# Kernel optimization log

Measured on AMD Instinct MI355X. Metric: run time of the kernel, lower is better.

Reference implementation:

```python
import jax, jax.numpy as jnp
import numpy as np

B, S, D, H = 4, 2048, 512, 8
EPS = 1e-5


def setup_inputs() -> dict:
    key = jax.random.key(0)
    ks = jax.random.split(key, 8)
    s = lambda fan_in: 1.0 / np.sqrt(fan_in)
    return {
        "x": jax.random.normal(ks[0], (B, S, D), jnp.float32),
        "ln_w": jnp.ones((D,), jnp.float32),
        "ln_b": jnp.zeros((D,), jnp.float32),
        "q_w": jax.random.normal(ks[1], (D, D * H), jnp.float32) * s(D),
        "q_b": jnp.zeros((D * H,), jnp.float32),
        "k_w": jax.random.normal(ks[2], (D, D * H), jnp.float32) * s(D),
        "k_b": jnp.zeros((D * H,), jnp.float32),
        "v_w": jax.random.normal(ks[3], (D, D * H), jnp.float32) * s(D),
        "v_b": jnp.zeros((D * H,), jnp.float32),
        "o_w": jax.random.normal(ks[4], (D * H, D), jnp.float32) * s(D * H),
        "o_b": jnp.zeros((D,), jnp.float32),
    }


def reference(x, ln_w, ln_b, q_w, q_b, k_w, k_b, v_w, v_b, o_w, o_b):
    # LayerNorm over last dim
    mu = jnp.mean(x, axis=-1, keepdims=True)
    var = jnp.var(x, axis=-1, keepdims=True)
    xn = (x - mu) * jax.lax.rsqrt(var + EPS) * ln_w + ln_b

    def proj(w, b):  # [B,S,D] -> [B,H,S,D] (head_dim == D per the module)
        y = xn @ w + b
        return y.reshape(B, S, H, D).transpose(0, 2, 1, 3)

    q, k, v = proj(q_w, q_b), proj(k_w, k_b), proj(v_w, v_b)
    scale = D ** (-0.5)
    att = jnp.einsum("bhqd,bhkd->bhqk", q, k) * scale
    att = jax.nn.softmax(att, axis=-1)  # dropout p=0 -> identity
    out = jnp.einsum("bhqk,bhkd->bhqd", att, v)
    out = out.transpose(0, 2, 1, 3).reshape(B, S, H * D)
    return out @ o_w + o_b
```

## Files before the change

### kernel.cpp

```cpp
#include <hip/hip_runtime.h>

typedef unsigned short u16;
typedef unsigned int u32;
typedef long long i64;
typedef __attribute__((ext_vector_type(4))) float f32x4;
typedef __attribute__((ext_vector_type(8))) __bf16 bf16x8;

#define DEVI static __device__ __forceinline__

constexpr int kB = 4, kS = 2048, kD = 512, kH = 8;
constexpr int kND = kD * kH;
constexpr int kBS = kB * kS;
constexpr int kNQK = 2 * kND;
constexpr int kNQKV = 3 * kND;
constexpr float kScale = 0.044194173824159216f;

DEVI u16 f2bf(float f) {
  u32 u = __builtin_bit_cast(u32, f);
  return (u16)((u + 0x7fffu + ((u >> 16) & 1u)) >> 16);
}
DEVI float bf2f(u16 h) { return __builtin_bit_cast(float, (u32)h << 16); }

DEVI f32x4 mfma16(bf16x8 a, bf16x8 b, f32x4 c) {
  return __builtin_amdgcn_mfma_f32_16x16x32_bf16(a, b, c, 0, 0, 0);
}

DEVI void gld16(const u16* g, u16* l) {
  __builtin_amdgcn_global_load_lds(
      (const __attribute__((address_space(1))) void*)g,
      (__attribute__((address_space(3))) void*)l, 16, 0, 0);
}

__global__ void k_zero(float* __restrict__ p, int n) {
  int i = blockIdx.x * 256 + threadIdx.x;
  if (i < n) p[i] = 0.0f;
}

__global__ void k_cat2(const float* __restrict__ a, const float* __restrict__ b,
                       float* __restrict__ o) {
  int i = blockIdx.x * 256 + threadIdx.x;
  if (i < kND) o[i] = a[i];
  else if (i < 2 * kND) o[i] = b[i - kND];
}

__global__ __launch_bounds__(256) void k_red4(const float* __restrict__ p,
                                              const float* __restrict__ bias,
                                              float* __restrict__ out, int NP) {
  const int i = blockIdx.x * 256 + threadIdx.x;
  const float4* pv = reinterpret_cast<const float4*>(p);
  const float4 a = pv[i], b = pv[i + NP], c = pv[i + 2 * NP],
               d = pv[i + 3 * NP];
  const float4 bv = reinterpret_cast<const float4*>(bias)[i & 127];
  float4 r;
  r.x = a.x + b.x + c.x + d.x + bv.x;
  r.y = a.y + b.y + c.y + d.y + bv.y;
  r.z = a.z + b.z + c.z + d.z + bv.z;
  r.w = a.w + b.w + c.w + d.w + bv.w;
  reinterpret_cast<float4*>(out)[i] = r;
}

__global__ __launch_bounds__(256) void k_ln(const float* __restrict__ x,
                                            const float* __restrict__ lw,
                                            const float* __restrict__ lb,
                                            u16* __restrict__ xn) {
  const int lane = threadIdx.x & 63;
  const int row = (blockIdx.x << 2) + (threadIdx.x >> 6);
  const float4* xp = reinterpret_cast<const float4*>(x + (size_t)row * kD);
  float4 a = xp[lane * 2], b = xp[lane * 2 + 1];
  float s = a.x + a.y + a.z + a.w + b.x + b.y + b.z + b.w;
  float ss = a.x * a.x + a.y * a.y + a.z * a.z + a.w * a.w +
             b.x * b.x + b.y * b.y + b.z * b.z + b.w * b.w;
#pragma unroll
  for (int m = 1; m < 64; m <<= 1) {
    s += __shfl_xor(s, m, 64);
    ss += __shfl_xor(ss, m, 64);
  }
  const float mean = s * (1.0f / kD);
  const float var = ss * (1.0f / kD) - mean * mean;
  const float rstd = rsqrtf(fmaxf(var, 0.0f) + 1e-5f);
  const float4* wp = reinterpret_cast<const float4*>(lw);
  const float4* bp = reinterpret_cast<const float4*>(lb);
  float4 w0 = wp[lane * 2], w1 = wp[lane * 2 + 1];
  float4 b0 = bp[lane * 2], b1 = bp[lane * 2 + 1];
  float o0 = (a.x - mean) * rstd * w0.x + b0.x;
  float o1 = (a.y - mean) * rstd * w0.y + b0.y;
  float o2 = (a.z - mean) * rstd * w0.z + b0.z;
  float o3 = (a.w - mean) * rstd * w0.w + b0.w;
  float o4 = (b.x - mean) * rstd * w1.x + b1.x;
  float o5 = (b.y - mean) * rstd * w1.y + b1.y;
  float o6 = (b.z - mean) * rstd * w1.z + b1.z;
  float o7 = (b.w - mean) * rstd * w1.w + b1.w;
  uint4 st = make_uint4((u32)f2bf(o0) | ((u32)f2bf(o1) << 16),
                        (u32)f2bf(o2) | ((u32)f2bf(o3) << 16),
                        (u32)f2bf(o4) | ((u32)f2bf(o5) << 16),
                        (u32)f2bf(o6) | ((u32)f2bf(o7) << 16));
  *reinterpret_cast<uint4*>(xn + (size_t)row * kD + lane * 8) = st;
}

__global__ void k_wt(const float* __restrict__ in, u16* __restrict__ out,
                     int R, int C) {
  __shared__ float t[32][33];
  const int tx = threadIdx.x, ty = threadIdx.y;
  const int c0 = blockIdx.x << 5, r0 = blockIdx.y << 5;
#pragma unroll
  for (int i = 0; i < 4; i++)
    t[ty + 8 * i][tx] = in[(size_t)(r0 + ty + 8 * i) * C + c0 + tx];
  __syncthreads();
#pragma unroll
  for (int i = 0; i < 4; i++)
    out[(size_t)(c0 + ty + 8 * i) * R + r0 + tx] = f2bf(t[tx][ty + 8 * i]);
}

__global__ void k_vt(const u16* __restrict__ V, u16* __restrict__ VT, int ldv,
                     i64 sVz, i64 sVzH, i64 sTz) {
  const int z = blockIdx.z;
  V += (size_t)((i64)z * sVz + (i64)(z >> 3) * sVzH);
  VT += (size_t)((i64)z * sTz);
  __shared__ u16 t[32][33];
  const int tx = threadIdx.x, ty = threadIdx.y;
  const int s0 = blockIdx.x << 5, d0 = blockIdx.y << 5;
#pragma unroll
  for (int i = 0; i < 4; i++)
    t[ty + 8 * i][tx] = V[(size_t)(s0 + ty + 8 * i) * ldv + d0 + tx];
  __syncthreads();
#pragma unroll
  for (int i = 0; i < 4; i++)
    VT[(size_t)(d0 + ty + 8 * i) * kS + s0 + tx] = t[tx][ty + 8 * i];
}

template <int EPI, int BN>
DEVI void gemm_body(const u16* __restrict__ A, int lda, i64 sAz, i64 sAzH,
                    const u16* __restrict__ Bt, int ldb, i64 sBz, i64 sBzH,
                    void* __restrict__ Cb, int ldc, i64 sCz, i64 sCzH, int K,
                    const float* __restrict__ bias, float* __restrict__ lbase,
                    i64 sLz) {
  constexpr int NF = BN / 32;
  constexpr int BHALF = BN / 2;
  const int z = blockIdx.z;
  A += (size_t)((i64)z * sAz + (i64)(z >> 3) * sAzH);
  Bt += (size_t)((i64)z * sBz + (i64)(z >> 3) * sBzH);
  const i64 czoff = (i64)z * sCz + (i64)(z >> 3) * sCzH;
  float* lrow = lbase + (size_t)z * sLz;

  __shared__ __align__(16) u16 smem[8192 + 2 * BN * 32];
  u16* Asb = smem;
  u16* Bsb = smem + 8192;

  const int tid = threadIdx.x;
  const int lane = tid & 63, wid = tid >> 6;
  const int g = lane >> 4, lr = lane & 15;
  const int wr = wid >> 1, wc = wid & 1;
  const int m0 = blockIdx.x << 7, n0 = blockIdx.y * BN;

  const int scol = (((lane & 3) ^ ((lane >> 2) & 3)) << 3);
  const int srowA = (wid << 5) + (lane >> 2);
  const int srowB = (BN == 128) ? srowA : (wid << 4) + (lane >> 2);
  const u16* agp0 = A + (size_t)(m0 + srowA) * lda + scol;
  const u16* agp1 = A + (size_t)(m0 + srowA + 16) * lda + scol;
  const u16* bgp0 = Bt + (size_t)(n0 + srowB) * ldb + scol;
  const u16* bgp1 = Bt + (size_t)(n0 + srowB + 16) * ldb + scol;

  f32x4 acc[4][NF] = {};

  auto stage = [&](int ks, int buf) {
    const int ko = ks << 5;
    u16* ab = Asb + (buf << 12) + (wid << 10);
    gld16(agp0 + ko, ab);
    gld16(agp1 + ko, ab + 512);
    if constexpr (BN == 128) {
      u16* bb = Bsb + (buf << 12) + (wid << 10);
      gld16(bgp0 + ko, bb);
      gld16(bgp1 + ko, bb + 512);
    } else {
      u16* bb = Bsb + buf * (BN * 32) + (wid << 9);
      gld16(bgp0 + ko, bb);
    }
  };

  const int gx8 = ((g ^ (lr & 3)) << 3);

  const int nsteps = K >> 5;
  stage(0, 0);
  for (int ks = 0; ks < nsteps; ++ks) {
    const int cur = ks & 1;
    __syncthreads();
    if (ks + 1 < nsteps) stage(ks + 1, cur ^ 1);
    bf16x8 af[4], bfr[NF];
#pragma unroll
    for (int m = 0; m < 4; m++)
      af[m] = *reinterpret_cast<const bf16x8*>(
          &Asb[(cur << 12) + (wr * 64 + m * 16 + lr) * 32 + gx8]);
#pragma unroll
    for (int n = 0; n < NF; n++)
      bfr[n] = *reinterpret_cast<const bf16x8*>(
          &Bsb[cur * (BN * 32) + (wc * BHALF + n * 16 + lr) * 32 + gx8]);
#pragma unroll
    for (int m = 0; m < 4; m++)
#pragma unroll
      for (int n = 0; n < NF; n++)
        acc[m][n] = mfma16(af[m], bfr[n], acc[m][n]);
  }

  const int crow0 = m0 + wr * 64;
  const int ccol0 = n0 + wc * BHALF;

  if constexpr (EPI == 0) {
    u16* C16 = (u16*)Cb + (size_t)czoff;
#pragma unroll
    for (int n = 0; n < NF; n++) {
      const int col = ccol0 + n * 16 + lr;
      const float bv = bias[col];
#pragma unroll
      for (int m = 0; m < 4; m++)
#pragma unroll
        for (int j = 0; j < 4; j++) {
          const int row = crow0 + m * 16 + (g << 2) + j;
          C16[(size_t)row * ldc + col] = f2bf(acc[m][n][j] + bv);
        }
    }
  } else if constexpr (EPI == 1 || EPI == 4 || EPI == 6) {
    float* C32 = (float*)Cb + (size_t)czoff;
#pragma unroll
    for (int n = 0; n < NF; n++) {
      const int col = ccol0 + n * 16 + lr;
      const float bv = (EPI == 1) ? bias[col] : 0.0f;
#pragma unroll
      for (int m = 0; m < 4; m++)
#pragma unroll
        for (int j = 0; j < 4; j++) {
          const int row = crow0 + m * 16 + (g << 2) + j;
          float v = acc[m][n][j] + bv;
          if constexpr (EPI == 4) v += C32[(size_t)row * ldc + col];
          C32[(size_t)row * ldc + col] = v;
        }
    }
  } else if constexpr (EPI == 2) {
    u16* C16 = (u16*)Cb + (size_t)czoff;
#pragma unroll
    for (int m = 0; m < 4; m++) {
      float rsum[4] = {0.f, 0.f, 0.f, 0.f};
#pragma unroll
      for (int n = 0; n < NF; n++) {
        const int col = ccol0 + n * 16 + lr;
#pragma unroll
        for (int j = 0; j < 4; j++) {
          const float p = __expf(acc[m][n][j] * kScale);
          const u16 pb = f2bf(p);
          C16[(size_t)(crow0 + m * 16 + (g << 2) + j) * ldc + col] = pb;
          rsum[j] += bf2f(pb);
        }
      }
#pragma unroll
      for (int j = 0; j < 4; j++) {
        float r = rsum[j];
        r += __shfl_xor(r, 1, 64);
        r += __shfl_xor(r, 2, 64);
        r += __shfl_xor(r, 4, 64);
        r += __shfl_xor(r, 8, 64);
        if (lr == 0) atomicAdd(&lrow[crow0 + m * 16 + (g << 2) + j], r);
      }
    }
  } else if constexpr (EPI == 3) {
    u16* C16 = (u16*)Cb + (size_t)czoff;
#pragma unroll
    for (int m = 0; m < 4; m++)
#pragma unroll
      for (int j = 0; j < 4; j++) {
        const int row = crow0 + m * 16 + (g << 2) + j;
        const float inv = 1.0f / lrow[row];
#pragma unroll
        for (int n = 0; n < NF; n++) {
          const int col = ccol0 + n * 16 + lr;
          C16[(size_t)row * ldc + col] = f2bf(acc[m][n][j] * inv);
        }
      }
  } else if constexpr (EPI == 5) {
    u16* T = smem;
    __syncthreads();
#pragma unroll
    for (int n = 0; n < NF; n++) {
      const int cl = wc * BHALF + n * 16 + lr;
      const float bv = bias[n0 + cl];
#pragma unroll
      for (int m = 0; m < 4; m++) {
        const int rlb = wr * 64 + m * 16 + (g << 2);
#pragma unroll
        for (int j = 0; j < 4; j++) {
          const int rl = rlb + j;
          T[cl * 128 + ((((rl >> 3) ^ (cl & 7)) << 3) | (rl & 7))] =
              f2bf(acc[m][n][j] + bv);
        }
      }
    }
    __syncthreads();
    const int zb = ((m0 >> 11) << 3) + (n0 >> 9);
    u16* VT = (u16*)Cb + (size_t)zb * kD * kS + (size_t)(n0 & 511) * kS +
              (m0 & 2047);
#pragma unroll
    for (int p = 0; p < 8; p++) {
      const int dl = p * 16 + (tid >> 4);
      const int r8 = tid & 15;
      *reinterpret_cast<uint4*>(VT + (size_t)dl * kS + (r8 << 3)) =
          *reinterpret_cast<const uint4*>(
              &T[dl * 128 + ((r8 ^ (dl & 7)) << 3)]);
    }
  }
}

#define GEMM_ARGS                                                             \
  const u16 *A, int lda, i64 sAz, i64 sAzH, const u16 *Bt, int ldb, i64 sBz,  \
      i64 sBzH, void *Cb, int ldc, i64 sCz, i64 sCzH, int K,                  \
      const float *bias, float *lbase, i64 sLz
#define GEMM_PASS A, lda, sAz, sAzH, Bt, ldb, sBz, sBzH, Cb, ldc, sCz, sCzH, \
      K, bias, lbase, sLz

__global__ __launch_bounds__(256) void k_qkproj(GEMM_ARGS) {
  gemm_body<0, 128>(GEMM_PASS);
}
__global__ __launch_bounds__(256) void k_vproj(GEMM_ARGS) {
  gemm_body<5, 128>(GEMM_PASS);
}
__global__ __launch_bounds__(256) void k_qkt(GEMM_ARGS) {
  gemm_body<2, 128>(GEMM_PASS);
}
__global__ __launch_bounds__(256) void k_pv(GEMM_ARGS) {
  gemm_body<3, 64>(GEMM_PASS);
}
__global__ __launch_bounds__(256) void k_pv128(GEMM_ARGS) {
  gemm_body<3, 128>(GEMM_PASS);
}
__global__ __launch_bounds__(256) void k_osplit(GEMM_ARGS) {
  gemm_body<6, 64>(GEMM_PASS);
}
__global__ __launch_bounds__(256) void k_oproj(GEMM_ARGS) {
  gemm_body<1, 128>(GEMM_PASS);
}
__global__ __launch_bounds__(256) void k_oacc(GEMM_ARGS) {
  gemm_body<4, 128>(GEMM_PASS);
}

extern "C" void kernel_launch(void* const* d_in, const int* in_sizes, int n_in,
                              void* d_out, int out_size, void* d_ws,
                              size_t ws_size, hipStream_t stream) {
  const float* x = (const float*)d_in[0];
  const float* ln_w = (const float*)d_in[1];
  const float* ln_b = (const float*)d_in[2];
  const float* q_w = (const float*)d_in[3];
  const float* q_b = (const float*)d_in[4];
  const float* k_w = (const float*)d_in[5];
  const float* k_b = (const float*)d_in[6];
  const float* v_w = (const float*)d_in[7];
  const float* v_b = (const float*)d_in[8];
  const float* o_w = (const float*)d_in[9];
  const float* o_b = (const float*)d_in[10];
  float* out = (float*)d_out;

  constexpr size_t SZ_XN = (size_t)kBS * kD * 2;
  constexpr size_t SZ_QKVT = (size_t)kNQKV * kD * 2;
  constexpr size_t SZ_OWT = (size_t)kND * kD * 2;
  constexpr size_t SZ_CB = (size_t)kNQK * 4;
  constexpr size_t SZ_LB = (size_t)32 * kS * 4;
  constexpr size_t SZ_QK1 = (size_t)kS * kNQK * 2;
  constexpr size_t SZ_VT1 = (size_t)8 * kD * kS * 2;
  constexpr size_t SZ_S1 = (size_t)8 * kS * kS * 2;
  constexpr size_t SZ_TIER = SZ_QK1 + SZ_VT1 + SZ_S1;
  constexpr size_t SZ_AO = (size_t)kBS * kND * 2;
  constexpr size_t SZ_S = (size_t)kS * kS * 2;
  constexpr size_t SZ_H = (size_t)kBS * kD * 2;
  constexpr size_t SZ_BH = (size_t)kS * kD * 2;
  const size_t common = SZ_XN + SZ_QKVT + SZ_OWT + SZ_CB + SZ_LB;

  char* p = (char*)d_ws;
  auto alloc = [&](size_t bytes) {
    char* r = p;
    p += (bytes + 255) & ~(size_t)255;
    return r;
  };
  auto fits = [&](size_t extra) { return common + extra + 8192 <= ws_size; };

  int nb = 0, plan = -1, zc = 0;
  if (fits(4 * SZ_TIER)) nb = 4;
  else if (fits(2 * SZ_TIER)) nb = 2;
  else if (fits(1 * SZ_TIER)) nb = 1;
  else if (fits(4 * SZ_H + SZ_AO + 4 * SZ_S)) { plan = 1; zc = 4; }
  else if (fits(4 * SZ_H + SZ_AO + 1 * SZ_S)) { plan = 1; zc = 1; }
  else if (fits(5 * SZ_H + 4 * SZ_S)) { plan = 2; zc = 4; }
  else if (fits(5 * SZ_H + 1 * SZ_S)) { plan = 2; zc = 1; }
  else { plan = 3; zc = 1; }

  u16* xn = (u16*)alloc(SZ_XN);
  u16* qkvT = (u16*)alloc(SZ_QKVT);
  u16* owT = (u16*)alloc(SZ_OWT);
  float* cbias = (float*)alloc(SZ_CB);
  float* lbuf = (float*)alloc(SZ_LB);

  u16* kwT = qkvT + (size_t)kND * kD;
  u16* vwT = qkvT + (size_t)2 * kND * kD;

  k_zero<<<dim3(256), 256, 0, stream>>>(lbuf, 32 * kS);
  k_ln<<<dim3(kBS / 4), 256, 0, stream>>>(x, ln_w, ln_b, xn);
  dim3 tb(32, 8);
  k_wt<<<dim3(kND / 32, kD / 32), tb, 0, stream>>>(q_w, qkvT, kD, kND);
  k_wt<<<dim3(kND / 32, kD / 32), tb, 0, stream>>>(k_w, kwT, kD, kND);
  k_wt<<<dim3(kND / 32, kD / 32), tb, 0, stream>>>(v_w, vwT, kD, kND);
  k_wt<<<dim3(kD / 32, kND / 32), tb, 0, stream>>>(o_w, owT, kND, kD);

  const i64 sS = (i64)kS * kS;

  if (nb > 0) {
    u16* QKg = (u16*)alloc((size_t)nb * SZ_QK1);
    u16* VTg = (u16*)alloc((size_t)nb * SZ_VT1);
    u16* Sb = (u16*)alloc((size_t)nb * SZ_S1);
    u16* AOg = QKg;
    float* Pb = (float*)Sb;

    k_cat2<<<dim3(kNQK / 256), 256, 0, stream>>>(q_b, k_b, cbias);

    const i64 sHiA = (i64)kS * kNQK - 8 * kD;
    const i64 sHiAO = (i64)kS * kND - 8 * kD;
    const int zc8 = nb * 8;

    for (int g = 0; g < kB; g += nb) {
      const u16* xb = xn + (size_t)g * kS * kD;
      k_qkproj<<<dim3(nb * kS / 128, kNQK / 128), 256, 0, stream>>>(
          xb, kD, 0, 0, qkvT, kD, 0, 0, QKg, kNQK, 0, 0, kD, cbias, nullptr,
          0);
      k_vproj<<<dim3(nb * kS / 128, kND / 128), 256, 0, stream>>>(
          xb, kD, 0, 0, vwT, kD, 0, 0, VTg, 0, 0, 0, kD, v_b, nullptr, 0);

      float* lr0 = lbuf + (size_t)g * 8 * kS;
      k_qkt<<<dim3(16, 16, zc8), 256, 0, stream>>>(
          QKg, kNQK, kD, sHiA, QKg + kND, kNQK, kD, sHiA, Sb, kS, sS, 0, kD,
          nullptr, lr0, kS);
      k_pv128<<<dim3(16, 4, zc8), 256, 0, stream>>>(
          Sb, kS, sS, 0, VTg, kS, (i64)kD * kS, 0, AOg, kND, kD, sHiAO, kS,
          nullptr, lr0, kS);
      k_osplit<<<dim3(nb * kS / 128, kD / 64, 4), 256, 0, stream>>>(
          AOg, kND, 1024, 0, owT, kND, 1024, 0, Pb, kD, (i64)nb * kS * kD, 0,
          1024, nullptr, nullptr, 0);
      k_red4<<<dim3(nb * kS * kD / 4 / 256), 256, 0, stream>>>(
          Pb, o_b, out + (size_t)g * kS * kD, nb * kS * kD / 4);
    }
  } else if (plan == 1 || plan == 2) {
    u16* Qh = (u16*)alloc(SZ_H);
    u16* Kh = (u16*)alloc(SZ_H);
    u16* Vh = (u16*)alloc(SZ_H);
    u16* VTh = (u16*)alloc(SZ_H);
    u16* AO = (u16*)alloc(plan == 1 ? SZ_AO : SZ_H);
    u16* Sb = (u16*)alloc((size_t)zc * SZ_S);
    const int aold = (plan == 1) ? kND : kD;

    for (int h = 0; h < kH; h++) {
      const u16* qwh = qkvT + (size_t)h * kD * kD;
      const u16* kwh = kwT + (size_t)h * kD * kD;
      const u16* vwh = vwT + (size_t)h * kD * kD;
      k_qkproj<<<dim3(64, 4), 256, 0, stream>>>(xn, kD, 0, 0, qwh, kD, 0, 0,
                                                Qh, kD, 0, 0, kD, q_b + h * kD,
                                                nullptr, 0);
      k_qkproj<<<dim3(64, 4), 256, 0, stream>>>(xn, kD, 0, 0, kwh, kD, 0, 0,
                                                Kh, kD, 0, 0, kD, k_b + h * kD,
                                                nullptr, 0);
      k_qkproj<<<dim3(64, 4), 256, 0, stream>>>(xn, kD, 0, 0, vwh, kD, 0, 0,
                                                Vh, kD, 0, 0, kD, v_b + h * kD,
                                                nullptr, 0);
      k_vt<<<dim3(64, 16, 4), tb, 0, stream>>>(Vh, VTh, kD, (i64)kS * kD, 0,
                                               (i64)kD * kS);
      u16* AOh = (plan == 1) ? AO + (size_t)h * kD : AO;
      const i64 sAO = (plan == 1) ? (i64)kS * kND : (i64)kS * kD;
      for (int b0 = 0; b0 < kB; b0 += zc) {
        float* lr0 = lbuf + (size_t)(h * 4 + b0) * kS;
        k_qkt<<<dim3(16, 16, zc), 256, 0, stream>>>(
            Qh + (size_t)b0 * kS * kD, kD, (i64)kS * kD, 0,
            Kh + (size_t)b0 * kS * kD, kD, (i64)kS * kD, 0, Sb, kS, sS, 0, kD,
            nullptr, lr0, kS);
        k_pv<<<dim3(16, 8, zc), 256, 0, stream>>>(
            Sb, kS, sS, 0, VTh + (size_t)b0 * kD * kS, kS, (i64)kD * kS, 0,
            AOh + (size_t)b0 * kS * aold, aold, sAO, 0, kS, nullptr, lr0, kS);
      }
      if (plan == 2) {
        if (h == 0)
          k_oproj<<<dim3(64, 4), 256, 0, stream>>>(
              AO, kD, 0, 0, owT + (size_t)h * kD, kND, 0, 0, out, kD, 0, 0, kD,
              o_b, nullptr, 0);
        else
          k_oacc<<<dim3(64, 4), 256, 0, stream>>>(
              AO, kD, 0, 0, owT + (size_t)h * kD, kND, 0, 0, out, kD, 0, 0, kD,
              nullptr, nullptr, 0);
      }
    }
    if (plan == 1)
      k_oproj<<<dim3(64, 4), 256, 0, stream>>>(AO, kND, 0, 0, owT, kND, 0, 0,
                                               out, kD, 0, 0, kND, o_b,
                                               nullptr, 0);
  } else {
    u16* Qbh = (u16*)alloc(SZ_BH);
    u16* Kbh = (u16*)alloc(SZ_BH);
    u16* Vbh = (u16*)alloc(SZ_BH);
    u16* VTbh = (u16*)alloc(SZ_BH);
    u16* AObh = (u16*)alloc(SZ_BH);
    u16* Sb = (u16*)alloc(SZ_S);

    for (int b = 0; b < kB; b++)
      for (int h = 0; h < kH; h++) {
        const u16* xb = xn + (size_t)b * kS * kD;
        k_qkproj<<<dim3(16, 4), 256, 0, stream>>>(
            xb, kD, 0, 0, qkvT + (size_t)h * kD * kD, kD, 0, 0, Qbh, kD, 0, 0,
            kD, q_b + h * kD, nullptr, 0);
        k_qkproj<<<dim3(16, 4), 256, 0, stream>>>(
            xb, kD, 0, 0, kwT + (size_t)h * kD * kD, kD, 0, 0, Kbh, kD, 0, 0,
            kD, k_b + h * kD, nullptr, 0);
        k_qkproj<<<dim3(16, 4), 256, 0, stream>>>(
            xb, kD, 0, 0, vwT + (size_t)h * kD * kD, kD, 0, 0, Vbh, kD, 0, 0,
            kD, v_b + h * kD, nullptr, 0);
        k_vt<<<dim3(64, 16, 1), tb, 0, stream>>>(Vbh, VTbh, kD, 0, 0, 0);
        float* lr0 = lbuf + (size_t)(b * 8 + h) * kS;
        k_qkt<<<dim3(16, 16, 1), 256, 0, stream>>>(
            Qbh, kD, 0, 0, Kbh, kD, 0, 0, Sb, kS, 0, 0, kD, nullptr, lr0, 0);
        k_pv<<<dim3(16, 8, 1), 256, 0, stream>>>(
            Sb, kS, 0, 0, VTbh, kS, 0, 0, AObh, kD, 0, 0, kS, nullptr, lr0, 0);
        float* outb = out + (size_t)b * kS * kD;
        if (h == 0)
          k_oproj<<<dim3(16, 4), 256, 0, stream>>>(
              AObh, kD, 0, 0, owT, kND, 0, 0, outb, kD, 0, 0, kD, o_b, nullptr,
              0);
        else
          k_oacc<<<dim3(16, 4), 256, 0, stream>>>(
              AObh, kD, 0, 0, owT + (size_t)h * kD, kND, 0, 0, outb, kD, 0, 0,
              kD, nullptr, nullptr, 0);
      }
  }
}
```

Measured before the change: 686.1 us.

## Fuse Q/K/V projections into one launch and stage GEMM epilogues through LDS

Merges the separate QK and V projection kernels into a single GEMM launch over the concatenated QKV weight. Column tiles in the V range write a transposed V layout; the combined bias is built by a three-way concat kernel. The QK projection, QK^T/exp and PV epilogues now stage their bf16 tiles through swizzled shared memory and write 16-byte coalesced rows instead of scattered 2-byte stores. This adds extra barriers and LDS traffic in each epilogue, and it reuses the lbase argument to carry the VT pointer.

New measurement: 684.7 us. About the same (-0.2%).

```diff
diff --git a/kernel.cpp b/kernel.cpp
--- a/kernel.cpp
+++ b/kernel.cpp
@@ -36,11 +36,12 @@
   if (i < n) p[i] = 0.0f;
 }
 
-__global__ void k_cat2(const float* __restrict__ a, const float* __restrict__ b,
-                       float* __restrict__ o) {
+__global__ void k_cat3(const float* __restrict__ a, const float* __restrict__ b,
+                       const float* __restrict__ c, float* __restrict__ o) {
   int i = blockIdx.x * 256 + threadIdx.x;
   if (i < kND) o[i] = a[i];
   else if (i < 2 * kND) o[i] = b[i - kND];
+  else if (i < 3 * kND) o[i] = c[i - 2 * kND];
 }
 
 __global__ __launch_bounds__(256) void k_red4(const float* __restrict__ p,
@@ -128,6 +129,11 @@
     VT[(size_t)(d0 + ty + 8 * i) * kS + s0 + tx] = t[tx][ty + 8 * i];
 }
 
+DEVI int tidx(int row, int col) {
+  return row * 128 + ((((col >> 3) ^ (((row >> 2) & 3) << 1)) << 3) |
+                      (col & 7));
+}
+
 template <int EPI, int BN>
 DEVI void gemm_body(const u16* __restrict__ A, int lda, i64 sAz, i64 sAzH,
                     const u16* __restrict__ Bt, int ldb, i64 sBz, i64 sBzH,
@@ -204,19 +210,67 @@
   const int crow0 = m0 + wr * 64;
   const int ccol0 = n0 + wc * BHALF;
 
-  if constexpr (EPI == 0) {
-    u16* C16 = (u16*)Cb + (size_t)czoff;
-#pragma unroll
-    for (int n = 0; n < NF; n++) {
-      const int col = ccol0 + n * 16 + lr;
-      const float bv = bias[col];
-#pragma unroll
-      for (int m = 0; m < 4; m++)
-#pragma unroll
-        for (int j = 0; j < 4; j++) {
-          const int row = crow0 + m * 16 + (g << 2) + j;
-          C16[(size_t)row * ldc + col] = f2bf(acc[m][n][j] + bv);
+  auto flush128 = [&](u16* C16, int ld) {
+    __syncthreads();
+#pragma unroll
+    for (int it = 0; it < 8; ++it) {
+      const int r = it * 16 + (tid >> 4);
+      const int b = tid & 15;
+      const int sb = b ^ (((r >> 2) & 3) << 1);
+      *reinterpret_cast<uint4*>(C16 + (size_t)(m0 + r) * ld + n0 + b * 8) =
+          *reinterpret_cast<const uint4*>(&smem[r * 128 + sb * 8]);
+    }
+  };
+
+  if constexpr (EPI == 0 || EPI == 7) {
+    const bool qkpart = (EPI == 0) || (n0 < kNQK);
+    if (qkpart) {
+      __syncthreads();
+#pragma unroll
+      for (int n = 0; n < NF; n++) {
+        const int cl = wc * BHALF + n * 16 + lr;
+        const float bv = bias[n0 + cl];
+#pragma unroll
+        for (int m = 0; m < 4; m++)
+#pragma unroll
+          for (int j = 0; j < 4; j++) {
+            const int rl = wr * 64 + m * 16 + (g << 2) + j;
+            smem[tidx(rl, cl)] = f2bf(acc[m][n][j] + bv);
+          }
+      }
+      u16* C16 = (u16*)Cb + (size_t)czoff;
+      flush128(C16, ldc);
+    } else {
+      u16* T = smem;
+      __syncthreads();
+      const int ndl = n0 - kNQK;
+#pragma unroll
+      for (int n = 0; n < NF; n++) {
+        const int cl = wc * BHALF + n * 16 + lr;
+        const float bv = bias[n0 + cl];
+#pragma unroll
+        for (int m = 0; m < 4; m++) {
+          const int rlb = wr * 64 + m * 16 + (g << 2);
+#pragma unroll
+          for (int j = 0; j < 4; j++) {
+            const int rl = rlb + j;
+            T[cl * 128 + ((((rl >> 3) ^ (cl & 7)) << 3) | (rl & 7))] =
+                f2bf(acc[m][n][j] + bv);
+          }
         }
+      }
+      __syncthreads();
+      const int zb = ((m0 >> 11) << 3) + (ndl >> 9);
+      u16* VT = (u16*)lbase + (size_t)zb * kD * kS +
+                (size_t)(ndl & 511) * kS + (m0 & 2047);
+#pragma unroll
+      for (int p = 0; p < 8; p++) {
+        const int dl = p * 16 + (tid >> 4);
+        const int r8 = tid & 15;
+        *reinterpret_cast<uint4*>(VT + (size_t)dl * kS + (r8 << 3)) =
+            *reinterpret_cast<const uint4*>(
+                &T[dl * 128 + ((r8 ^ (dl & 7)) << 3)]);
+      }
     }
   } else if constexpr (EPI == 1 || EPI == 4 || EPI == 6) {
     float* C32 = (float*)Cb + (size_t)czoff;
@@ -235,18 +289,19 @@
         }
     }
   } else if constexpr (EPI == 2) {
-    u16* C16 = (u16*)Cb + (size_t)czoff;
+    __syncthreads();
 #pragma unroll
     for (int m = 0; m < 4; m++) {
       float rsum[4] = {0.f, 0.f, 0.f, 0.f};
 #pragma unroll
       for (int n = 0; n < NF; n++) {
-        const int col = ccol0 + n * 16 + lr;
+        const int cl = wc * BHALF + n * 16 + lr;
 #pragma unroll
         for (int j = 0; j < 4; j++) {
+          const int rl = wr * 64 + m * 16 + (g << 2) + j;
           const float p = __expf(acc[m][n][j] * kScale);
           const u16 pb = f2bf(p);
-          C16[(size_t)(crow0 + m * 16 + (g << 2) + j) * ldc + col] = pb;
+          smem[tidx(rl, cl)] = pb;
           rsum[j] += bf2f(pb);
         }
       }
@@ -260,49 +315,39 @@
         if (lr == 0) atomicAdd(&lrow[crow0 + m * 16 + (g << 2) + j], r);
       }
     }
+    u16* C16 = (u16*)Cb + (size_t)czoff;
+    flush128(C16, ldc);
   } else if constexpr (EPI == 3) {
-    u16* C16 = (u16*)Cb + (size_t)czoff;
-#pragma unroll
-    for (int m = 0; m < 4; m++)
-#pragma unroll
-      for (int j = 0; j < 4; j++) {
-        const int row = crow0 + m * 16 + (g << 2) + j;
-        const float inv = 1.0f / lrow[row];
-#pragma unroll
-        for (int n = 0; n < NF; n++) {
-          const int col = ccol0 + n * 16 + lr;
-          C16[(size_t)row * ldc + col] = f2bf(acc[m][n][j] * inv);
+    if constexpr (BN == 128) {
+      __syncthreads();
+#pragma unroll
+      for (int m = 0; m < 4; m++)
+#pragma unroll
+        for (int j = 0; j < 4; j++) {
+          const int rl = wr * 64 + m * 16 + (g << 2) + j;
+          const float inv = 1.0f / lrow[m0 + rl];
+#pragma unroll
+          for (int n = 0; n < NF; n++) {
+            const int cl = wc * BHALF + n * 16 + lr;
+            smem[tidx(rl, cl)] = f2bf(acc[m][n][j] * inv);
+          }
         }
-      }
-  } else if constexpr (EPI == 5) {
-    u16* T = smem;
-    __syncthreads();
-#pragma unroll
-    for (int n = 0; n < NF; n++) {
-      const int cl = wc * BHALF + n * 16 + lr;
-      const float bv = bias[n0 + cl];
-#pragma unroll
-      for (int m = 0; m < 4; m++) {
-        const int rlb = wr * 64 + m * 16 + (g << 2);
+      u16* C16 = (u16*)Cb + (size_t)czoff;
+      flush128(C16, ldc);
+    } else {
+      u16* C16 = (u16*)Cb + (size_t)czoff;
+#pragma unroll
+      for (int m = 0; m < 4; m++)
 #pragma unroll
         for (int j = 0; j < 4; j++) {
-          const int rl = rlb + j;
-          T[cl * 128 + ((((rl >> 3) ^ (cl & 7)) << 3) | (rl & 7))] =
-              f2bf(acc[m][n][j] + bv);
+          const int row = crow0 + m * 16 + (g << 2) + j;
+          const float inv = 1.0f / lrow[row];
+#pragma unroll
+          for (int n = 0; n < NF; n++) {
+            const int col = ccol0 + n * 16 + lr;
+            C16[(size_t)row * ldc + col] = f2bf(acc[m][n][j] * inv);
+          }
         }
-      }
-    }
-    __syncthreads();
-    const int zb = ((m0 >> 11) << 3) + (n0 >> 9);
-    u16* VT = (u16*)Cb + (size_t)zb * kD * kS + (size_t)(n0 & 511) * kS +
-              (m0 & 2047);
-#pragma unroll
-    for (int p = 0; p < 8; p++) {
-      const int dl = p * 16 + (tid >> 4);
-      const int r8 = tid & 15;
-      *reinterpret_cast<uint4*>(VT + (size_t)dl * kS + (r8 << 3)) =
-          *reinterpret_cast<const uint4*>(
-              &T[dl * 128 + ((r8 ^ (dl & 7)) << 3)]);
     }
   }
 }
@@ -317,8 +362,8 @@
 __global__ __launch_bounds__(256) void k_qkproj(GEMM_ARGS) {
   gemm_body<0, 128>(GEMM_PASS);
 }
-__global__ __launch_bounds__(256) void k_vproj(GEMM_ARGS) {
-  gemm_body<5, 128>(GEMM_PASS);
+__global__ __launch_bounds__(256) void k_qkvproj(GEMM_ARGS) {
+  gemm_body<7, 128>(GEMM_PASS);
 }
 __global__ __launch_bounds__(256) void k_qkt(GEMM_ARGS) {
   gemm_body<2, 128>(GEMM_PASS);
@@ -358,7 +403,7 @@
   constexpr size_t SZ_XN = (size_t)kBS * kD * 2;
   constexpr size_t SZ_QKVT = (size_t)kNQKV * kD * 2;
   constexpr size_t SZ_OWT = (size_t)kND * kD * 2;
-  constexpr size_t SZ_CB = (size_t)kNQK * 4;
+  constexpr size_t SZ_CB = (size_t)kNQKV * 4;
   constexpr size_t SZ_LB = (size_t)32 * kS * 4;
   constexpr size_t SZ_QK1 = (size_t)kS * kNQK * 2;
   constexpr size_t SZ_VT1 = (size_t)8 * kD * kS * 2;
@@ -414,7 +459,7 @@
     u16* AOg = QKg;
     float* Pb = (float*)Sb;
 
-    k_cat2<<<dim3(kNQK / 256), 256, 0, stream>>>(q_b, k_b, cbias);
+    k_cat3<<<dim3(kNQKV / 256), 256, 0, stream>>>(q_b, k_b, v_b, cbias);
 
     const i64 sHiA = (i64)kS * kNQK - 8 * kD;
     const i64 sHiAO = (i64)kS * kND - 8 * kD;
@@ -422,11 +467,9 @@
 
     for (int g = 0; g < kB; g += nb) {
       const u16* xb = xn + (size_t)g * kS * kD;
-      k_qkproj<<<dim3(nb * kS / 128, kNQK / 128), 256, 0, stream>>>(
-          xb, kD, 0, 0, qkvT, kD, 0, 0, QKg, kNQK, 0, 0, kD, cbias, nullptr,
-          0);
-      k_vproj<<<dim3(nb * kS / 128, kND / 128), 256, 0, stream>>>(
-          xb, kD, 0, 0, vwT, kD, 0, 0, VTg, 0, 0, 0, kD, v_b, nullptr, 0);
+      k_qkvproj<<<dim3(nb * kS / 128, kNQKV / 128), 256, 0, stream>>>(
+          xb, kD, 0, 0, qkvT, kD, 0, 0, QKg, kNQK, 0, 0, kD, cbias,
+          (float*)VTg, 0);
 
       float* lr0 = lbuf + (size_t)g * 8 * kS;
       k_qkt<<<dim3(16, 16, zc8), 256, 0, stream>>>(
```
